# Kernel tuning notes

Measured on AMD Instinct MI355X. Metric: run time of the kernel, lower is better.

## Reference

```python
import jax, jax.numpy as jnp
from jax import lax
import numpy as np

B, L, DIM = 4, 4096, 512
H, HD = 8, 64            # num_heads, head_dim
CHUNK = 128              # chunk size for chunk-recurrent lightning attention
LN_EPS = 1e-5


def _slopes(h):
    # _build_slope_tensor for power-of-2 heads: 2^(-8*(i+1)/h), cast through fp16
    s = np.array([2.0 ** (-8.0 * (i + 1) / h) for i in range(h)], dtype=np.float32)
    return jnp.asarray(s.astype(np.float16).astype(np.float32))  # [h]


def _layernorm(x, w, b):
    mu = jnp.mean(x, axis=-1, keepdims=True)
    var = jnp.mean((x - mu) ** 2, axis=-1, keepdims=True)
    return (x - mu) * lax.rsqrt(var + LN_EPS) * w + b


def _rmsnorm(x, gamma):
    # F.normalize(x, dim=-1) * sqrt(d) * gamma ; gamma [h,1,d] broadcasts over [b,h,l,d]
    n = x / jnp.maximum(jnp.linalg.norm(x, axis=-1, keepdims=True), 1e-12)
    return n * (HD ** 0.5) * gamma


def _lightning_attn(q, k, v, slopes):
    # q,k,v: [b,h,L,d]; causal linear attention with per-head decay exp(-s*(t-j))
    b, h, l, d = q.shape
    nc = l // CHUNK
    s = slopes[:, None, None]                      # [h,1,1]
    r = jnp.arange(CHUNK, dtype=q.dtype)
    diff = r[:, None] - r[None, :]                 # [C,C]
    Dintra = jnp.where(diff >= 0, jnp.exp(-s * diff), 0.0)   # [h,C,C]
    q_dec = jnp.exp(-slopes[:, None] * r[None, :])           # [h,C] decay from chunk start
    k_dec = jnp.exp(-slopes[:, None] * (CHUNK - r[None, :])) # [h,C] decay to next chunk start
    c_dec = jnp.exp(-slopes * CHUNK)                         # [h]

    def to_chunks(t):
        return t.reshape(b, h, nc, CHUNK, d).transpose(2, 0, 1, 3, 4)  # [nc,b,h,C,d]

    qc, kc, vc = to_chunks(q), to_chunks(k), to_chunks(v)

    def step(kv, inp):
        qi, ki, vi = inp                                       # [b,h,C,d]
        scores = jnp.einsum('bhid,bhjd->bhij', qi, ki) * Dintra[None]
        intra = jnp.einsum('bhij,bhjd->bhid', scores, vi)
        inter = jnp.einsum('bhcd,bhde->bhce', qi * q_dec[None, :, :, None], kv)
        kv = kv * c_dec[None, :, None, None] + jnp.einsum(
            'bhcd,bhce->bhde', ki * k_dec[None, :, :, None], vi)
        return kv, intra + inter

    kv0 = jnp.zeros((b, h, d, d), q.dtype)
    _, out = lax.scan(step, kv0, (qc, kc, vc))                 # [nc,b,h,C,d]
    return out.transpose(1, 2, 0, 3, 4).reshape(b, h, l, d)


def setup_inputs() -> dict:
    key = jax.random.key(0)
    ks = jax.random.split(key, 8)
    std = lambda fan_in: 1.0 / np.sqrt(fan_in)
    return {
        'x': jax.random.normal(ks[0], (B, L, DIM), jnp.float32),
        'ln1_w': jnp.ones((DIM,), jnp.float32),
        'ln1_b': jnp.zeros((DIM,), jnp.float32),
        'rel_bias': 0.02 * jax.random.normal(ks[1], (1, L, DIM), jnp.float32),
        'qkv_w': std(DIM) * jax.random.normal(ks[2], (3 * DIM, DIM), jnp.float32),
        'qkv_b': jnp.zeros((3 * DIM,), jnp.float32),
        'gq': jnp.ones((H, 1, HD), jnp.float32) / (HD ** 0.5),
        'gk': jnp.ones((H, 1, HD), jnp.float32) / (HD ** 0.5),
        'proj_w': std(DIM) * jax.random.normal(ks[3], (DIM, DIM), jnp.float32),
        'proj_b': jnp.zeros((DIM,), jnp.float32),
        'ln2_w': jnp.ones((DIM,), jnp.float32),
        'ln2_b': jnp.zeros((DIM,), jnp.float32),
        'fc1_w': std(DIM) * jax.random.normal(ks[4], (4 * DIM, DIM), jnp.float32),
        'fc1_b': jnp.zeros((4 * DIM,), jnp.float32),
        'fc2_w': std(4 * DIM) * jax.random.normal(ks[5], (DIM, 4 * DIM), jnp.float32),
        'fc2_b': jnp.zeros((DIM,), jnp.float32),
    }


def reference(x, ln1_w, ln1_b, rel_bias, qkv_w, qkv_b, gq, gk,
              proj_w, proj_b, ln2_w, ln2_b, fc1_w, fc1_b, fc2_w, fc2_b):
    slopes = _slopes(H)
    b, l, c = x.shape
    shortcut = x
    h = _layernorm(x, ln1_w, ln1_b)
    # --- LightningAttention ---
    h = h + rel_bias
    qkv = (h @ qkv_w.T + qkv_b).reshape(b, l, 3, H, HD).transpose(2, 0, 3, 1, 4)
    q, k, v = qkv[0], qkv[1], qkv[2]                     # [b,h,l,d]
    q = _rmsnorm(q * (HD ** -0.5), gq)
    k = _rmsnorm(k, gk)
    o = _lightning_attn(q, k, v, slopes)                 # [b,h,l,d]
    o = o.reshape(b, l, c)                               # faithful to source: reshape, no head transpose
    o = o @ proj_w.T + proj_b
    x = o + shortcut
    # --- MLP ---
    shortcut = x
    h = _layernorm(x, ln2_w, ln2_b)
    h = jax.nn.gelu(h @ fc1_w.T + fc1_b, approximate=False)
    h = h @ fc2_w.T + fc2_b
    return h + shortcut
```

## Files before the change

### kernel.cpp

```cpp
#include <hip/hip_runtime.h>
#include <math.h>

typedef unsigned short u16;
typedef __bf16 bf16x8 __attribute__((ext_vector_type(8)));
typedef float f32x4 __attribute__((ext_vector_type(4)));

#define DEVI static __device__ __forceinline__

DEVI float b2f(u16 u) { union { unsigned int i; float f; } w; w.i = ((unsigned int)u) << 16; return w.f; }
DEVI u16 f2b(float f) {
  union { float f; unsigned int i; } w; w.f = f;
  unsigned int r = (w.i + 0x7FFFu + ((w.i >> 16) & 1u)) >> 16;
  return (u16)r;
}

DEVI float fast_gelu(float v) {
  float z = fabsf(v) * 0.70710678118654752f;
  float t = __builtin_amdgcn_rcpf(1.0f + 0.3275911f * z);
  float p = ((((1.061405429f * t - 1.453152027f) * t + 1.421413741f) * t
              - 0.284496736f) * t + 0.254829592f) * t;
  float er = 1.0f - p * __expf(-z * z);
  er = (v < 0.0f) ? -er : er;
  return 0.5f * v * (1.0f + er);
}

__global__ void conv_f2b_kernel(const float* __restrict__ s, u16* __restrict__ d, int n) {
  int i = blockIdx.x * 256 + threadIdx.x;
  int st = gridDim.x * 256;
  for (; i < n; i += st) d[i] = f2b(s[i]);
}

template<int ADD_REL>
__global__ __launch_bounds__(256) void ln_kernel(
    const float* __restrict__ x, const float* __restrict__ w, const float* __restrict__ bb,
    const float* __restrict__ rel, u16* __restrict__ out) {
  int row = blockIdx.x;
  int t = threadIdx.x;
  const float* xr = x + (size_t)row * 512;
  float v0 = xr[t], v1 = xr[t + 256];
  float s = v0 + v1, ss = v0 * v0 + v1 * v1;
#pragma unroll
  for (int o = 32; o > 0; o >>= 1) { s += __shfl_down(s, o); ss += __shfl_down(ss, o); }
  __shared__ float rs[4], rss[4];
  int lane = t & 63, wid = t >> 6;
  if (lane == 0) { rs[wid] = s; rss[wid] = ss; }
  __syncthreads();
  s = rs[0] + rs[1] + rs[2] + rs[3];
  ss = rss[0] + rss[1] + rss[2] + rss[3];
  float mu = s * (1.0f / 512.0f);
  float inv = rsqrtf(ss * (1.0f / 512.0f) - mu * mu + 1e-5f);
  float o0 = (v0 - mu) * inv * w[t] + bb[t];
  float o1 = (v1 - mu) * inv * w[t + 256] + bb[t + 256];
  if (ADD_REL) {
    const float* rr = rel + (size_t)(row & 4095) * 512;
    o0 += rr[t]; o1 += rr[t + 256];
  }
  u16* orow = out + (size_t)row * 512;
  orow[t] = f2b(o0);
  orow[t + 256] = f2b(o1);
}

template<int EPI>
__global__ __launch_bounds__(256) void gemm_bt_kernel(
    const u16* __restrict__ A, const u16* __restrict__ W,
    const float* __restrict__ bias, int M, int N, int K, int NBN,
    const float* __restrict__ resid, u16* __restrict__ outb,
    u16* __restrict__ q_out, u16* __restrict__ k_out, u16* __restrict__ v_out,
    float* __restrict__ outf, const float* __restrict__ gq, const float* __restrict__ gk) {
  __shared__ u16 As[128 * 32];
  __shared__ u16 Bs[128 * 32];
  int nwg = gridDim.x, wg = blockIdx.x;
  int wgs = (wg & 7) * (nwg >> 3) + (wg >> 3);
  int bn = wgs % NBN, bm = wgs / NBN;
  int m0 = bm * 128, n0 = bn * 128;
  int t = threadIdx.x, lane = t & 63, wid = t >> 6;
  int wr = (wid >> 1) * 64, wc = (wid & 1) * 64;
  int fr = lane & 15, fk = (lane >> 4) * 8;
  int srow = wid * 32 + (lane >> 2);
  int scol = (lane & 3) * 8;
  const u16* gA = A + (size_t)(m0 + srow) * K + scol;
  const u16* gB = W + (size_t)(n0 + srow) * K + scol;
  u16* lA = &As[wid * 1024];
  u16* lB = &Bs[wid * 1024];
  f32x4 acc[4][4] = {};
  for (int k0 = 0; k0 < K; k0 += 32) {
    __builtin_amdgcn_global_load_lds(gA + k0,          lA,       16, 0, 0);
    __builtin_amdgcn_global_load_lds(gA + k0 + 16 * K, lA + 512, 16, 0, 0);
    __builtin_amdgcn_global_load_lds(gB + k0,          lB,       16, 0, 0);
    __builtin_amdgcn_global_load_lds(gB + k0 + 16 * K, lB + 512, 16, 0, 0);
    __syncthreads();
    bf16x8 af[4], bfr[4];
#pragma unroll
    for (int i = 0; i < 4; ++i) af[i] = *(const bf16x8*)&As[(wr + i * 16 + fr) * 32 + fk];
#pragma unroll
    for (int j = 0; j < 4; ++j) bfr[j] = *(const bf16x8*)&Bs[(wc + j * 16 + fr) * 32 + fk];
#pragma unroll
    for (int i = 0; i < 4; ++i)
#pragma unroll
      for (int j = 0; j < 4; ++j)
        acc[i][j] = __builtin_amdgcn_mfma_f32_16x16x32_bf16(af[i], bfr[j], acc[i][j], 0, 0, 0);
    __syncthreads();
  }
  int fq = lane >> 4;
  if (EPI == 0) {
    int nb = n0 + wc;
    int which = nb >> 9, head = (nb >> 6) & 7;
    const float* gg = (which == 0) ? gq : gk;
#pragma unroll
    for (int i = 0; i < 4; ++i) {
#pragma unroll
      for (int jj = 0; jj < 4; ++jj) {
        int gm = m0 + wr + i * 16 + fq * 4 + jj;
        int b = gm >> 12, l = gm & 4095;
        float v[4]; float ssum = 0.f;
#pragma unroll
        for (int j = 0; j < 4; ++j) {
          v[j] = acc[i][j][jj] + bias[nb + j * 16 + fr];
          ssum += v[j] * v[j];
        }
        u16* dst = (which == 0) ? q_out : (which == 1) ? k_out : v_out;
        size_t rowbase = (((size_t)(b * 8 + head) * 4096) + l) * 64;
        if (which == 2) {
#pragma unroll
          for (int j = 0; j < 4; ++j) dst[rowbase + j * 16 + fr] = f2b(v[j]);
        } else {
#pragma unroll
          for (int o = 1; o < 16; o <<= 1) ssum += __shfl_xor(ssum, o);
          float inv = 8.0f / fmaxf(sqrtf(ssum), 1e-12f);
#pragma unroll
          for (int j = 0; j < 4; ++j)
            dst[rowbase + j * 16 + fr] = f2b(v[j] * inv * gg[head * 64 + j * 16 + fr]);
        }
      }
    }
  } else {
#pragma unroll
    for (int i = 0; i < 4; ++i) {
#pragma unroll
      for (int j = 0; j < 4; ++j) {
#pragma unroll
        for (int jj = 0; jj < 4; ++jj) {
          int gm = m0 + wr + i * 16 + fq * 4 + jj;
          int gn = n0 + wc + j * 16 + fr;
          float v = acc[i][j][jj] + bias[gn];
          if (EPI == 1) {
            size_t idx = (size_t)gm * 512 + gn;
            outf[idx] = v + resid[idx];
          } else if (EPI == 2) {
            outb[(size_t)gm * (size_t)N + gn] = f2b(fast_gelu(v));
          } else {
            size_t idx = (size_t)gm * 512 + gn;
            outf[idx] = v + resid[idx];
          }
        }
      }
    }
  }
}

__global__ __launch_bounds__(256) void attn_kv_kernel(
    const u16* __restrict__ k, const u16* __restrict__ v, float* __restrict__ P) {
  constexpr int LT = 136;
  __shared__ __align__(16) u16 kT_s[64 * LT];
  __shared__ __align__(16) u16 vT_s[64 * LT];
  __shared__ float kdec[128];
  int bid = blockIdx.x;
  int bh = bid >> 5;
  float sl = exp2f(-(float)((bh & 7) + 1));
  int t = threadIdx.x, lane = t & 63, wid = t >> 6;
  for (int i = t; i < 128; i += 256) kdec[i] = expf(-sl * (float)(128 - i));
  const u16* kb = k + (size_t)bid * 8192;
  const u16* vb = v + (size_t)bid * 8192;
  __syncthreads();
  int fr = lane & 15, fk = (lane >> 4) * 8, fq = lane >> 4;
#pragma unroll
  for (int i = 0; i < 16; ++i) {
    int seg = t + i * 256;
    int j = seg >> 5, dd = (seg & 31) * 2;
    unsigned int kp = *(const unsigned int*)&kb[(size_t)j * 64 + dd];
    float kd = kdec[j];
    kT_s[dd * LT + j] = f2b(b2f((u16)(kp & 0xFFFFu)) * kd);
    kT_s[(dd + 1) * LT + j] = f2b(b2f((u16)(kp >> 16)) * kd);
    unsigned int vp = *(const unsigned int*)&vb[(size_t)j * 64 + dd];
    vT_s[dd * LT + j] = (u16)(vp & 0xFFFFu);
    vT_s[(dd + 1) * LT + j] = (u16)(vp >> 16);
  }
  __syncthreads();
  f32x4 accKV[4] = {};
#pragma unroll
  for (int kk = 0; kk < 4; ++kk) {
    bf16x8 akt = *(const bf16x8*)&kT_s[(wid * 16 + fr) * LT + kk * 32 + fk];
#pragma unroll
    for (int j = 0; j < 4; ++j) {
      bf16x8 bvt = *(const bf16x8*)&vT_s[(j * 16 + fr) * LT + kk * 32 + fk];
      accKV[j] = __builtin_amdgcn_mfma_f32_16x16x32_bf16(akt, bvt, accKV[j], 0, 0, 0);
    }
  }
  float* PT = (float*)kT_s;
  __syncthreads();
#pragma unroll
  for (int j = 0; j < 4; ++j)
#pragma unroll
    for (int jj = 0; jj < 4; ++jj) {
      int dd = wid * 16 + fq * 4 + jj;
      int e = j * 16 + fr;
      PT[e * 68 + dd] = accKV[j][jj];
    }
  __syncthreads();
  float* Pg = P + (size_t)bid * 4096;
  int e = t >> 2, d0 = (t & 3) * 16;
#pragma unroll
  for (int g = 0; g < 4; ++g) {
    f32x4 val = *(const f32x4*)&PT[e * 68 + d0 + g * 4];
    *(f32x4*)&Pg[(size_t)e * 64 + d0 + g * 4] = val;
  }
}

__global__ __launch_bounds__(256) void attn_scan_kernel(
    const float* __restrict__ P, u16* __restrict__ kvst) {
  int bh = blockIdx.x, t = threadIdx.x;
  float sl = exp2f(-(float)((bh & 7) + 1));
  float cdec = expf(-sl * 128.0f);
  float kv[16];
#pragma unroll
  for (int i = 0; i < 16; ++i) kv[i] = 0.f;
  for (int c = 0; c < 32; ++c) {
    size_t off = (((size_t)bh * 32 + c) * 4096) + (size_t)t * 16;
    union { u16 st[16]; uint4 v4[4]; } u;
#pragma unroll
    for (int i = 0; i < 16; ++i) u.st[i] = f2b(kv[i]);
    *(uint4*)&kvst[off] = u.v4[0];
    *(uint4*)&kvst[off + 8] = u.v4[1];
#pragma unroll
    for (int g = 0; g < 4; ++g) {
      f32x4 p = *(const f32x4*)&P[off + g * 4];
#pragma unroll
      for (int e = 0; e < 4; ++e) kv[g * 4 + e] = cdec * kv[g * 4 + e] + p[e];
    }
  }
}

__global__ __launch_bounds__(256) void attn_out_kernel(
    const u16* __restrict__ q, const u16* __restrict__ k, const u16* __restrict__ v,
    const u16* __restrict__ kvst, u16* __restrict__ o) {
  constexpr int LQ = 72, LT = 136, LS = 136, LKV = 72;
  __shared__ __align__(16) u16 sm[31744];
  u16* q_s  = sm;
  u16* k_s  = sm + 9216;
  u16* vT_s = sm + 18432;
  u16* kvT_s = sm + 27136;
  u16* S_s  = sm;
  __shared__ float rowf[128], colf[128];
  int bid = blockIdx.x;
  int bh = bid >> 5;
  float sl = exp2f(-(float)((bh & 7) + 1));
  int t = threadIdx.x, lane = t & 63, wid = t >> 6;
  for (int i = t; i < 128; i += 256) {
    rowf[i] = expf(-sl * i);
    colf[i] = expf(sl * i);
  }
  const u16* qb = q + (size_t)bid * 8192;
  const u16* kb = k + (size_t)bid * 8192;
  const u16* vb = v + (size_t)bid * 8192;
  const u16* kvb = kvst + (size_t)bid * 4096;
  u16* ob = o + (size_t)bid * 8192;
  int fr = lane & 15, fk = (lane >> 4) * 8, fq = lane >> 4;
#pragma unroll
  for (int i = 0; i < 4; ++i) {
    int seg = t + i * 256;
    int r = seg >> 3, cc = (seg & 7) * 8;
    *(uint4*)&q_s[r * LQ + cc] = *(const uint4*)&qb[(size_t)r * 64 + cc];
    *(uint4*)&k_s[r * LQ + cc] = *(const uint4*)&kb[(size_t)r * 64 + cc];
  }
#pragma unroll
  for (int i = 0; i < 16; ++i) {
    int seg = t + i * 256;
    int j = seg >> 5, dd = (seg & 31) * 2;
    unsigned int vp = *(const unsigned int*)&vb[(size_t)j * 64 + dd];
    vT_s[dd * LT + j] = (u16)(vp & 0xFFFFu);
    vT_s[(dd + 1) * LT + j] = (u16)(vp >> 16);
  }
#pragma unroll
  for (int i = 0; i < 2; ++i) {
    int seg = t + i * 256;
    int e = seg >> 3, dd = (seg & 7) * 8;
    *(uint4*)&kvT_s[e * LKV + dd] = *(const uint4*)&kvb[(size_t)e * 64 + dd];
  }
  __syncthreads();
  f32x4 accS[2][8] = {};
  f32x4 accI[2][4] = {};
#pragma unroll
  for (int kk = 0; kk < 2; ++kk) {
    bf16x8 aq0 = *(const bf16x8*)&q_s[(wid * 32 + fr) * LQ + kk * 32 + fk];
    bf16x8 aq1 = *(const bf16x8*)&q_s[(wid * 32 + 16 + fr) * LQ + kk * 32 + fk];
#pragma unroll
    for (int j = 0; j < 8; ++j) {
      bf16x8 bk = *(const bf16x8*)&k_s[(j * 16 + fr) * LQ + kk * 32 + fk];
      accS[0][j] = __builtin_amdgcn_mfma_f32_16x16x32_bf16(aq0, bk, accS[0][j], 0, 0, 0);
      accS[1][j] = __builtin_amdgcn_mfma_f32_16x16x32_bf16(aq1, bk, accS[1][j], 0, 0, 0);
    }
#pragma unroll
    for (int j = 0; j < 4; ++j) {
      bf16x8 bkv = *(const bf16x8*)&kvT_s[(j * 16 + fr) * LKV + kk * 32 + fk];
      accI[0][j] = __builtin_amdgcn_mfma_f32_16x16x32_bf16(aq0, bkv, accI[0][j], 0, 0, 0);
      accI[1][j] = __builtin_amdgcn_mfma_f32_16x16x32_bf16(aq1, bkv, accI[1][j], 0, 0, 0);
    }
  }
  __syncthreads();
#pragma unroll
  for (int i = 0; i < 2; ++i)
#pragma unroll
    for (int j = 0; j < 8; ++j)
#pragma unroll
      for (int jj = 0; jj < 4; ++jj) {
        int si = wid * 32 + i * 16 + fq * 4 + jj;
        int sj = j * 16 + fr;
        float val = (si >= sj) ? accS[i][j][jj] * rowf[si] * colf[sj] : 0.0f;
        S_s[si * LS + sj] = f2b(val);
      }
  __syncthreads();
  f32x4 accO[2][4] = {};
#pragma unroll
  for (int kk = 0; kk < 4; ++kk) {
    bf16x8 as0 = *(const bf16x8*)&S_s[(wid * 32 + fr) * LS + kk * 32 + fk];
    bf16x8 as1 = *(const bf16x8*)&S_s[(wid * 32 + 16 + fr) * LS + kk * 32 + fk];
#pragma unroll
    for (int j = 0; j < 4; ++j) {
      bf16x8 bvt = *(const bf16x8*)&vT_s[(j * 16 + fr) * LT + kk * 32 + fk];
      accO[0][j] = __builtin_amdgcn_mfma_f32_16x16x32_bf16(as0, bvt, accO[0][j], 0, 0, 0);
      accO[1][j] = __builtin_amdgcn_mfma_f32_16x16x32_bf16(as1, bvt, accO[1][j], 0, 0, 0);
    }
  }
#pragma unroll
  for (int i = 0; i < 2; ++i)
#pragma unroll
    for (int j = 0; j < 4; ++j)
#pragma unroll
      for (int jj = 0; jj < 4; ++jj) {
        int li = wid * 32 + i * 16 + fq * 4 + jj;
        int e = j * 16 + fr;
        float val = accO[i][j][jj] + rowf[li] * accI[i][j][jj];
        ob[(size_t)li * 64 + e] = f2b(val);
      }
}

extern "C" void kernel_launch(void* const* d_in, const int* in_sizes, int n_in,
                              void* d_out, int out_size, void* d_ws, size_t ws_size,
                              hipStream_t stream) {
  const float* x      = (const float*)d_in[0];
  const float* ln1_w  = (const float*)d_in[1];
  const float* ln1_b  = (const float*)d_in[2];
  const float* rel    = (const float*)d_in[3];
  const float* qkv_w  = (const float*)d_in[4];
  const float* qkv_b  = (const float*)d_in[5];
  const float* gq     = (const float*)d_in[6];
  const float* gk     = (const float*)d_in[7];
  const float* proj_w = (const float*)d_in[8];
  const float* proj_b = (const float*)d_in[9];
  const float* ln2_w  = (const float*)d_in[10];
  const float* ln2_b  = (const float*)d_in[11];
  const float* fc1_w  = (const float*)d_in[12];
  const float* fc1_b  = (const float*)d_in[13];
  const float* fc2_w  = (const float*)d_in[14];
  const float* fc2_b  = (const float*)d_in[15];

  char* ws = (char*)d_ws;
  size_t off = 0;
  auto alloc = [&](size_t bytes) { char* p = ws + off; off += (bytes + 255) & ~(size_t)255; return p; };
  u16* w_qkv  = (u16*)alloc((size_t)1536 * 512 * 2);
  u16* w_proj = (u16*)alloc((size_t)512 * 512 * 2);
  u16* w_fc1  = (u16*)alloc((size_t)2048 * 512 * 2);
  u16* w_fc2  = (u16*)alloc((size_t)512 * 2048 * 2);
  u16* h_buf  = (u16*)alloc((size_t)16384 * 512 * 2);
  u16* q_buf  = (u16*)alloc((size_t)8388608 * 2);
  u16* k_buf  = (u16*)alloc((size_t)8388608 * 2);
  u16* v_buf  = (u16*)alloc((size_t)8388608 * 2);
  u16* o_buf  = (u16*)alloc((size_t)8388608 * 2);
  float* x2   = (float*)alloc((size_t)8388608 * 4);
  u16* mid    = q_buf;
  float* P_glob  = x2;
  u16*   kv_state = (u16*)(x2 + 4194304);

  conv_f2b_kernel<<<512, 256, 0, stream>>>(qkv_w, w_qkv, 1536 * 512);
  conv_f2b_kernel<<<512, 256, 0, stream>>>(proj_w, w_proj, 512 * 512);
  conv_f2b_kernel<<<512, 256, 0, stream>>>(fc1_w, w_fc1, 2048 * 512);
  conv_f2b_kernel<<<512, 256, 0, stream>>>(fc2_w, w_fc2, 512 * 2048);

  ln_kernel<1><<<16384, 256, 0, stream>>>(x, ln1_w, ln1_b, rel, h_buf);

  gemm_bt_kernel<0><<<1536, 256, 0, stream>>>(h_buf, w_qkv, qkv_b, 16384, 1536, 512, 12,
      nullptr, nullptr, q_buf, k_buf, v_buf, nullptr, gq, gk);

  attn_kv_kernel<<<1024, 256, 0, stream>>>(k_buf, v_buf, P_glob);
  attn_scan_kernel<<<32, 256, 0, stream>>>(P_glob, kv_state);
  attn_out_kernel<<<1024, 256, 0, stream>>>(q_buf, k_buf, v_buf, kv_state, o_buf);

  gemm_bt_kernel<1><<<512, 256, 0, stream>>>(o_buf, w_proj, proj_b, 16384, 512, 512, 4,
      x, nullptr, nullptr, nullptr, nullptr, x2, nullptr, nullptr);

  ln_kernel<0><<<16384, 256, 0, stream>>>(x2, ln2_w, ln2_b, nullptr, h_buf);

  gemm_bt_kernel<2><<<2048, 256, 0, stream>>>(h_buf, w_fc1, fc1_b, 16384, 2048, 512, 16,
      nullptr, mid, nullptr, nullptr, nullptr, nullptr, nullptr, nullptr);

  gemm_bt_kernel<3><<<512, 256, 0, stream>>>(mid, w_fc2, fc2_b, 16384, 512, 2048, 4,
      x2, nullptr, nullptr, nullptr, nullptr, (float*)d_out, nullptr, nullptr);

  (void)in_sizes; (void)n_in; (void)out_size; (void)ws_size;
}
```

Before: 290.4 us.

## Double-buffer GEMM LDS tiles and use sigmoid-based GELU approximation

```diff
diff --git a/kernel.cpp b/kernel.cpp
--- a/kernel.cpp
+++ b/kernel.cpp
@@ -15,13 +15,10 @@
 }
 
 DEVI float fast_gelu(float v) {
-  float z = fabsf(v) * 0.70710678118654752f;
-  float t = __builtin_amdgcn_rcpf(1.0f + 0.3275911f * z);
-  float p = ((((1.061405429f * t - 1.453152027f) * t + 1.421413741f) * t
-              - 0.284496736f) * t + 0.254829592f) * t;
-  float er = 1.0f - p * __expf(-z * z);
-  er = (v < 0.0f) ? -er : er;
-  return 0.5f * v * (1.0f + er);
+  float x2 = v * v;
+  float p = fmaf(0.10294357f, x2, 2.30215855f);
+  float ex = exp2f(-v * p);
+  return v * __builtin_amdgcn_rcpf(1.0f + ex);
 }
 
 __global__ void conv_f2b_kernel(const float* __restrict__ s, u16* __restrict__ d, int n) {
@@ -67,8 +64,8 @@
     const float* __restrict__ resid, u16* __restrict__ outb,
     u16* __restrict__ q_out, u16* __restrict__ k_out, u16* __restrict__ v_out,
     float* __restrict__ outf, const float* __restrict__ gq, const float* __restrict__ gk) {
-  __shared__ u16 As[128 * 32];
-  __shared__ u16 Bs[128 * 32];
+  __shared__ u16 As[2][128 * 32];
+  __shared__ u16 Bs[2][128 * 32];
   int nwg = gridDim.x, wg = blockIdx.x;
   int wgs = (wg & 7) * (nwg >> 3) + (wg >> 3);
   int bn = wgs % NBN, bm = wgs / NBN;
@@ -80,26 +77,34 @@
   int scol = (lane & 3) * 8;
   const u16* gA = A + (size_t)(m0 + srow) * K + scol;
   const u16* gB = W + (size_t)(n0 + srow) * K + scol;
-  u16* lA = &As[wid * 1024];
-  u16* lB = &Bs[wid * 1024];
   f32x4 acc[4][4] = {};
-  for (int k0 = 0; k0 < K; k0 += 32) {
+  auto STAGE = [&](int sel, int k0) {
+    u16* lA = &As[sel][wid * 1024];
+    u16* lB = &Bs[sel][wid * 1024];
     __builtin_amdgcn_global_load_lds(gA + k0,          lA,       16, 0, 0);
     __builtin_amdgcn_global_load_lds(gA + k0 + 16 * K, lA + 512, 16, 0, 0);
     __builtin_amdgcn_global_load_lds(gB + k0,          lB,       16, 0, 0);
     __builtin_amdgcn_global_load_lds(gB + k0 + 16 * K, lB + 512, 16, 0, 0);
-    __syncthreads();
+  };
+  STAGE(0, 0);
+  asm volatile("s_waitcnt vmcnt(0)" ::: "memory");
+  __builtin_amdgcn_s_barrier();
+  int cur = 0;
+  for (int k0 = 0; k0 < K; k0 += 32) {
+    if (k0 + 32 < K) STAGE(cur ^ 1, k0 + 32);
     bf16x8 af[4], bfr[4];
 #pragma unroll
-    for (int i = 0; i < 4; ++i) af[i] = *(const bf16x8*)&As[(wr + i * 16 + fr) * 32 + fk];
-#pragma unroll
-    for (int j = 0; j < 4; ++j) bfr[j] = *(const bf16x8*)&Bs[(wc + j * 16 + fr) * 32 + fk];
+    for (int i = 0; i < 4; ++i) af[i] = *(const bf16x8*)&As[cur][(wr + i * 16 + fr) * 32 + fk];
+#pragma unroll
+    for (int j = 0; j < 4; ++j) bfr[j] = *(const bf16x8*)&Bs[cur][(wc + j * 16 + fr) * 32 + fk];
 #pragma unroll
     for (int i = 0; i < 4; ++i)
 #pragma unroll
       for (int j = 0; j < 4; ++j)
         acc[i][j] = __builtin_amdgcn_mfma_f32_16x16x32_bf16(af[i], bfr[j], acc[i][j], 0, 0, 0);
-    __syncthreads();
+    asm volatile("s_waitcnt vmcnt(0)" ::: "memory");
+    __builtin_amdgcn_s_barrier();
+    cur ^= 1;
   }
   int fq = lane >> 4;
   if (EPI == 0) {
```

Result: faster. 280.0 us (-3.6%).
